# Performance work log

Hardware: AMD Instinct MI355X
Metric: run time of the kernel (lower is better)

The kernel has to match this reference:

```python
import jax, jax.numpy as jnp
import numpy as np
from jax import lax

B, V, C, D, H, W = 1, 5, 32, 48, 128, 160
RATIO = 8


def setup_inputs() -> dict:
    key = jax.random.key(0)
    k1, k2, k3 = jax.random.split(key, 3)
    features = jax.random.normal(k1, (V, B, C, H, W), jnp.float32)
    # proj_matrices[b, v, 0] = 4x4 extrinsic, proj_matrices[b, v, 1, :3, :3] = intrinsic K
    f = 200.0
    K = np.array([[f, 0.0, W / 2.0], [0.0, f, H / 2.0], [0.0, 0.0, 1.0]], np.float32)
    proj = np.zeros((B, V, 2, 4, 4), np.float32)
    for v in range(V):
        E = np.eye(4, dtype=np.float32)
        E[0, 3] = 2.0 * v  # horizontal baseline per source view
        proj[:, v, 0] = E
        P1 = np.eye(4, dtype=np.float32)
        P1[:3, :3] = K
        proj[:, v, 1] = P1
    proj_matrices = jnp.asarray(proj)
    depth_values = jnp.broadcast_to(jnp.linspace(425.0, 935.0, D, dtype=jnp.float32), (B, D))
    mask = jax.random.normal(k2, (B, 9 * RATIO * RATIO, H, W), jnp.float32)
    W_reg = jax.random.normal(k3, (1, C, 3, 3, 3), jnp.float32) * 0.05
    return {"features": features, "proj_matrices": proj_matrices,
            "depth_values": depth_values, "mask": mask, "W_reg": W_reg}


def _combine(p):
    # p: [B,2,4,4] -> K @ E[:3,:4] written into top 3 rows of extrinsic (as in source)
    top = jnp.einsum('bij,bjk->bik', p[:, 1, :3, :3], p[:, 0, :3, :4])
    return p[:, 0].at[:, :3, :4].set(top)


def _bilinear_sample(src, x, y):
    # src [B,C,H,W]; x,y [B,P] pixel coords; zeros padding, align_corners=True
    Bs, Cs, Hs, Ws = src.shape
    x0 = jnp.floor(x)
    y0 = jnp.floor(y)
    wx = x - x0
    wy = y - y0
    src_flat = src.reshape(Bs, Cs, Hs * Ws)

    def gather(xi, yi, w):
        valid = (xi >= 0) & (xi <= Ws - 1) & (yi >= 0) & (yi <= Hs - 1)
        xi_c = jnp.clip(xi, 0, Ws - 1).astype(jnp.int32)
        yi_c = jnp.clip(yi, 0, Hs - 1).astype(jnp.int32)
        idx = (yi_c * Ws + xi_c)[:, None, :]
        vals = jnp.take_along_axis(src_flat, jnp.broadcast_to(idx, (Bs, Cs, idx.shape[-1])), axis=2)
        return vals * (w * valid)[:, None, :]

    return (gather(x0, y0, (1 - wx) * (1 - wy)) + gather(x0 + 1, y0, wx * (1 - wy))
            + gather(x0, y0 + 1, (1 - wx) * wy) + gather(x0 + 1, y0 + 1, wx * wy))


def _homo_warp(src_fea, src_proj, ref_proj, depth_values):
    # faithful homo_warping2: project ref pixel grid at each depth hypothesis into src view
    Bs, Cs, Hs, Ws = src_fea.shape
    Dd = depth_values.shape[1]
    proj = jnp.einsum('bij,bjk->bik', src_proj, jnp.linalg.inv(ref_proj))
    rot = proj[:, :3, :3]
    trans = proj[:, :3, 3]
    ys, xs = jnp.meshgrid(jnp.arange(Hs, dtype=src_fea.dtype), jnp.arange(Ws, dtype=src_fea.dtype), indexing='ij')
    xyz = jnp.stack([xs.ravel(), ys.ravel(), jnp.ones(Hs * Ws, dtype=src_fea.dtype)])  # [3,HW]
    rot_xyz = jnp.einsum('bij,jp->bip', rot, xyz)  # [B,3,HW]
    pts = rot_xyz[:, :, None, :] * depth_values[:, None, :, None] + trans[:, :, None, None]  # [B,3,D,HW]
    gx = pts[:, 0] / pts[:, 2]
    gy = pts[:, 1] / pts[:, 2]
    warped = _bilinear_sample(src_fea, gx.reshape(Bs, -1), gy.reshape(Bs, -1))
    return warped.reshape(Bs, Cs, Dd, Hs, Ws)


def _convex_upsample(depth, mask, r):
    # depth [N,1,H,W], mask [N,9*r*r,H,W] -> [N, r*H, r*W]
    N, _, Hh, Ww = depth.shape
    m = jax.nn.softmax(mask.reshape(N, 1, 9, r, r, Hh, Ww), axis=2)
    dp = jnp.pad(depth, ((0, 0), (0, 0), (1, 1), (1, 1)))
    nb = jnp.stack([dp[:, :, dy:dy + Hh, dx:dx + Ww] for dy in range(3) for dx in range(3)], axis=2)
    up = jnp.sum(m * nb[:, :, :, None, None], axis=2)  # [N,1,r,r,H,W]
    up = up.transpose(0, 1, 4, 2, 5, 3)  # [N,1,H,r,W,r]
    return up.reshape(N, r * Hh, r * Ww)


def reference(features, proj_matrices, depth_values, mask, W_reg):
    num_views = features.shape[0]
    Dd = depth_values.shape[1]
    ref_proj = _combine(proj_matrices[:, 0])
    # variance cost-volume accumulation over views (ref volume broadcast along D)
    vsum = features[0][:, :, None, :, :]
    vsq = vsum ** 2
    for v in range(1, num_views):
        src_proj = _combine(proj_matrices[:, v])
        wv = _homo_warp(features[v], src_proj, ref_proj, depth_values)
        vsum = vsum + wv
        vsq = vsq + wv * wv
    variance = vsq / num_views - (vsum / num_views) ** 2  # [B,C,D,H,W]
    # cost regularization stand-in: 3x3x3 conv C->1, SAME padding
    pre = lax.conv_general_dilated(variance, W_reg, (1, 1, 1), 'SAME',
                                   dimension_numbers=('NCDHW', 'OIDHW', 'NCDHW'))[:, 0]
    prob = jax.nn.softmax(pre, axis=1)  # [B,D,H,W]
    depth = jnp.sum(prob * depth_values[:, :, None, None], axis=1)  # [B,H,W]
    # photometric confidence (no-grad path): sliding sum of 4 along D, pad (1,2)
    pd = jnp.pad(prob, ((0, 0), (1, 2), (0, 0), (0, 0)))
    sum4 = pd[:, 0:Dd] + pd[:, 1:Dd + 1] + pd[:, 2:Dd + 2] + pd[:, 3:Dd + 3]
    di = jnp.sum(prob * jnp.arange(Dd, dtype=prob.dtype)[None, :, None, None], axis=1).astype(jnp.int32)
    di = jnp.clip(di, 0, Dd - 1)
    conf = jax.lax.stop_gradient(jnp.take_along_axis(sum4, di[:, None], axis=1)[:, 0])
    depth_up = _convex_upsample(depth[:, None], mask, RATIO)
    return (depth_up, depth, conf)
```

## Files before the change

### kernel.cpp

```cpp
#include <hip/hip_runtime.h>
#include <hip/hip_bf16.h>


#define NV 5
#define NC 32
#define ND 48
#define NH 128
#define NW 160
#define HW (NH * NW)
#define DHW (ND * HW)

typedef __attribute__((ext_vector_type(2))) float f32x2;
typedef __attribute__((ext_vector_type(4))) float f32x4;
typedef __attribute__((ext_vector_type(2), aligned(4))) float f32x2u;

#define OFF_M      0
#define OFF_WF     256
#define OFF_DEPTHF 4096
#define OFF_PRE    86016
#define OFF_WV     4018176

__global__ void k_setup(const float* __restrict__ proj,
                        const float* __restrict__ wreg,
                        float* __restrict__ M, float* __restrict__ wf) {
  if (threadIdx.x != 0) return;
  double P[NV][2][4][4];
  for (int v = 0; v < NV; ++v)
    for (int m = 0; m < 2; ++m)
      for (int i = 0; i < 4; ++i)
        for (int j = 0; j < 4; ++j)
          P[v][m][i][j] = (double)proj[((v * 2 + m) * 4 + i) * 4 + j];
  double C[NV][4][4];
  for (int v = 0; v < NV; ++v) {
    for (int i = 0; i < 4; ++i)
      for (int j = 0; j < 4; ++j) C[v][i][j] = P[v][0][i][j];
    for (int i = 0; i < 3; ++i)
      for (int j = 0; j < 4; ++j) {
        double s = 0.0;
        for (int k = 0; k < 3; ++k) s += P[v][1][i][k] * P[v][0][k][j];
        C[v][i][j] = s;
      }
  }
  double a[4][8];
  for (int i = 0; i < 4; ++i)
    for (int j = 0; j < 4; ++j) { a[i][j] = C[0][i][j]; a[i][j + 4] = (i == j) ? 1.0 : 0.0; }
  for (int col = 0; col < 4; ++col) {
    int piv = col; double best = fabs(a[col][col]);
    for (int r = col + 1; r < 4; ++r) { double v = fabs(a[r][col]); if (v > best) { best = v; piv = r; } }
    if (piv != col)
      for (int j = 0; j < 8; ++j) { double t = a[col][j]; a[col][j] = a[piv][j]; a[piv][j] = t; }
    double pv = a[col][col];
    for (int j = 0; j < 8; ++j) a[col][j] /= pv;
    for (int r = 0; r < 4; ++r) if (r != col) {
      double f = a[r][col];
      for (int j = 0; j < 8; ++j) a[r][j] -= f * a[col][j];
    }
  }
  double inv[4][4];
  for (int i = 0; i < 4; ++i)
    for (int j = 0; j < 4; ++j) inv[i][j] = a[i][j + 4];
  for (int v = 1; v < NV; ++v) {
    float* m = M + (v - 1) * 12;
    for (int i = 0; i < 3; ++i) {
      double r[4] = {0, 0, 0, 0};
      for (int k = 0; k < 4; ++k) {
        double cv = C[v][i][k];
        for (int j = 0; j < 4; ++j) r[j] += cv * inv[k][j];
      }
      m[i * 3 + 0] = (float)r[0]; m[i * 3 + 1] = (float)r[1]; m[i * 3 + 2] = (float)r[2];
      m[9 + i] = (float)r[3];
    }
  }
  for (int c = 0; c < NC; ++c) {
    for (int t = 0; t < 27; ++t) wf[c * 28 + t] = wreg[c * 27 + t];
    wf[c * 28 + 27] = 0.f;
  }
}

__global__ __launch_bounds__(256) void k_warpvar(
    const float* __restrict__ feat,
    const float* __restrict__ depthv,
    const float* __restrict__ M,
    const float* __restrict__ wf,
    __hip_bfloat16* __restrict__ WV)
{
  int idx = blockIdx.x * 256 + threadIdx.x;
  int x = idx % NW;
  int t1 = idx / NW;
  int y = t1 % NH;
  int d = t1 / NH;
  int pix = y * NW + x;
  float xf = (float)x, yf = (float)y;
  float df = depthv[d];

  int   off[4];
  float wA[4], wB[4];
  bool any4 = false;

#pragma unroll
  for (int v = 0; v < 4; ++v) {
    const float* m = M + v * 12;
    float rx = m[0] * xf + m[1] * yf + m[2];
    float ry = m[3] * xf + m[4] * yf + m[5];
    float rz = m[6] * xf + m[7] * yf + m[8];
    float px = rx * df + m[9];
    float py = ry * df + m[10];
    float pz = rz * df + m[11];
    float gx = px / pz;
    float gy = py / pz;
    float y0 = floorf(gy);
    float wy = gy - y0;
    bool two = (wy == 0.f) || (wy == 1.f);
    any4 = any4 || !two;
    float rowf = (wy == 0.f) ? y0 : (y0 + 1.f);
    float x0 = floorf(gx);
    float wx = gx - x0;
    bool yok  = (rowf >= 0.f) && (rowf <= (float)(NH - 1));
    bool x0ok = (x0 >= 0.f) && (x0 <= (float)(NW - 1)) && yok;
    bool x1ok = (x0 + 1.f >= 0.f) && (x0 + 1.f <= (float)(NW - 1)) && yok;
    float rc = fminf(fmaxf(rowf, 0.f), (float)(NH - 1));
    float xc = fminf(fmaxf(x0, 0.f), (float)(NW - 1));
    int xi = (int)xc;
    int o = (int)rc * NW + xi;
    bool ddv = (o == HW - 1);
    bool sv  = (x0 >= 0.f) && (xi <= NW - 2);
    o -= ddv ? 1 : 0;
    float w0 = (1.f - wx) * (x0ok ? 1.f : 0.f);
    float w1 = wx * (x1ok ? 1.f : 0.f);
    float wsum = w0 + w1;
    wA[v] = ddv ? 0.f : (sv ? w0 : wsum);
    wB[v] = ddv ? wsum : (sv ? w1 : 0.f);
    off[v] = o;
  }

  f32x2 wv[14];
#pragma unroll
  for (int u = 0; u < 14; ++u) { wv[u].x = 0.f; wv[u].y = 0.f; }

  if (__builtin_expect(any4, 0)) {
    int cidx[16]; float cw[16];
#pragma unroll
    for (int v = 0; v < 4; ++v) {
      const float* m = M + v * 12;
      float rx = m[0] * xf + m[1] * yf + m[2];
      float ry = m[3] * xf + m[4] * yf + m[5];
      float rz = m[6] * xf + m[7] * yf + m[8];
      float px = rx * df + m[9];
      float py = ry * df + m[10];
      float pz = rz * df + m[11];
      float gx = px / pz;
      float gy = py / pz;
      float x0 = floorf(gx), y0 = floorf(gy);
      float wx = gx - x0, wy = gy - y0;
      float cxs[2] = {x0, x0 + 1.f}, cys[2] = {y0, y0 + 1.f};
      float wxs[2] = {1.f - wx, wx}, wys[2] = {1.f - wy, wy};
#pragma unroll
      for (int cy = 0; cy < 2; ++cy)
#pragma unroll
        for (int cx = 0; cx < 2; ++cx) {
          float fx = cxs[cx], fy = cys[cy];
          bool valid = (fx >= 0.f) && (fx <= (float)(NW - 1)) &&
                       (fy >= 0.f) && (fy <= (float)(NH - 1));
          float fxc = fminf(fmaxf(fx, 0.f), (float)(NW - 1));
          float fyc = fminf(fmaxf(fy, 0.f), (float)(NH - 1));
          int xi2 = (int)fxc, yi2 = (int)fyc;
          cidx[v * 4 + cy * 2 + cx] = yi2 * NW + xi2;
          cw[v * 4 + cy * 2 + cx] = wxs[cx] * wys[cy] * (valid ? 1.f : 0.f);
        }
    }
    for (int c = 0; c < NC; ++c) {
      float f0 = feat[c * HW + pix];
      float vs = f0, vq = f0 * f0;
#pragma unroll
      for (int v = 0; v < 4; ++v) {
        const float* fv = feat + ((v + 1) * NC + c) * HW;
        float val = cw[v * 4 + 0] * fv[cidx[v * 4 + 0]]
                  + cw[v * 4 + 1] * fv[cidx[v * 4 + 1]]
                  + cw[v * 4 + 2] * fv[cidx[v * 4 + 2]]
                  + cw[v * 4 + 3] * fv[cidx[v * 4 + 3]];
        vs += val;
        vq += val * val;
      }
      float var = vq * 0.2f - (vs * 0.2f) * (vs * 0.2f);
      const f32x2* wrow = (const f32x2*)(wf + c * 28);
      f32x2 vv; vv.x = var; vv.y = var;
#pragma unroll
      for (int u = 0; u < 14; ++u) wv[u] += wrow[u] * vv;
    }
  } else {
#pragma unroll
    for (int c = 0; c < NC; ++c) {
      float f0 = feat[c * HW + pix];
      float vs = f0, vq = f0 * f0;
#pragma unroll
      for (int v = 0; v < 4; ++v) {
        const float* fv = feat + ((v + 1) * NC + c) * HW;
        f32x2u e = *(const f32x2u*)(fv + off[v]);
        float val = wA[v] * e.x + wB[v] * e.y;
        vs += val;
        vq += val * val;
      }
      float var = vq * 0.2f - (vs * 0.2f) * (vs * 0.2f);
      const f32x2* wrow = (const f32x2*)(wf + c * 28);
      f32x2 vv; vv.x = var; vv.y = var;
#pragma unroll
      for (int u = 0; u < 14; ++u) wv[u] += wrow[u] * vv;
    }
  }

#pragma unroll
  for (int u = 0; u < 14; ++u) {
    int t0 = 2 * u;
    WV[t0 * DHW + idx] = __float2bfloat16(wv[u].x);
    if (t0 + 1 < 27) WV[(t0 + 1) * DHW + idx] = __float2bfloat16(wv[u].y);
  }
}

__global__ __launch_bounds__(256) void k_conv(const __hip_bfloat16* __restrict__ WV,
                                              float* __restrict__ pre) {
  int idx = blockIdx.x * 256 + threadIdx.x;
  int x = idx % NW;
  int t1 = idx / NW;
  int y = t1 % NH;
  int d = t1 / NH;
  float acc = 0.f;
#pragma unroll
  for (int dd = 0; dd < 3; ++dd) {
    int dp = d + dd - 1;
    bool dok = (dp >= 0) && (dp < ND);
    int dpc = min(max(dp, 0), ND - 1);
#pragma unroll
    for (int i = 0; i < 3; ++i) {
      int yp = y + i - 1;
      bool yok = (yp >= 0) && (yp < NH);
      int ypc = min(max(yp, 0), NH - 1);
#pragma unroll
      for (int j = 0; j < 3; ++j) {
        int xp = x + j - 1;
        bool xok = (xp >= 0) && (xp < NW);
        int xpc = min(max(xp, 0), NW - 1);
        int t = dd * 9 + i * 3 + j;
        float v = __bfloat162float(WV[t * DHW + dpc * HW + ypc * NW + xpc]);
        acc += (dok && yok && xok) ? v : 0.f;
      }
    }
  }
  pre[idx] = acc;
}

__global__ __launch_bounds__(256) void k_softmax(const float* __restrict__ pre,
                                                 const float* __restrict__ depthv,
                                                 float* __restrict__ depthf,
                                                 float* __restrict__ out_depth,
                                                 float* __restrict__ out_conf) {
  int p = blockIdx.x * 256 + threadIdx.x;
  float pr[ND];
  float m = -1e30f;
#pragma unroll
  for (int d = 0; d < ND; ++d) { pr[d] = pre[d * HW + p]; m = fmaxf(m, pr[d]); }
  float s = 0.f;
#pragma unroll
  for (int d = 0; d < ND; ++d) { pr[d] = expf(pr[d] - m); s += pr[d]; }
  float inv = 1.f / s;
  float dep = 0.f, ti = 0.f;
#pragma unroll
  for (int d = 0; d < ND; ++d) {
    float prob = pr[d] * inv;
    pr[d] = prob;
    dep += prob * depthv[d];
    ti += prob * (float)d;
  }
  int di = (int)ti;
  di = di < 0 ? 0 : (di > ND - 1 ? ND - 1 : di);
  float conf = 0.f;
#pragma unroll
  for (int d = 0; d < ND; ++d)
    conf += (d >= di - 1 && d <= di + 2) ? pr[d] : 0.f;
  depthf[p] = dep;
  out_depth[p] = dep;
  out_conf[p] = conf;
}

__global__ __launch_bounds__(256) void k_upsample(const float* __restrict__ mask,
                                                  const float* __restrict__ depthf,
                                                  float* __restrict__ out) {
  int idx = blockIdx.x * 256 + threadIdx.x;
  int x = idx % NW;
  int r = idx / NW;
  int y = r % NH;
  int dy = r / NH;
  int pix = y * NW + x;

  float dv[9];
#pragma unroll
  for (int k = 0; k < 9; ++k) {
    int ky = y + k / 3 - 1;
    int kx = x + k % 3 - 1;
    bool ok = (ky >= 0) && (ky < NH) && (kx >= 0) && (kx < NW);
    int kyc = min(max(ky, 0), NH - 1);
    int kxc = min(max(kx, 0), NW - 1);
    float t = depthf[kyc * NW + kxc];
    dv[k] = ok ? t : 0.f;
  }

  float res[8];
#pragma unroll
  for (int dx = 0; dx < 8; ++dx) {
    float mv[9];
    float mmax = -1e30f;
#pragma unroll
    for (int k = 0; k < 9; ++k) {
      mv[k] = mask[(size_t)(k * 64 + dy * 8 + dx) * HW + pix];
      mmax = fmaxf(mmax, mv[k]);
    }
    float s = 0.f, acc = 0.f;
#pragma unroll
    for (int k = 0; k < 9; ++k) {
      float e = expf(mv[k] - mmax);
      s += e;
      acc += e * dv[k];
    }
    res[dx] = acc / s;
  }

  float* op = out + (size_t)(y * 8 + dy) * (NW * 8) + x * 8;
  f32x4 lo, hi;
  lo.x = res[0]; lo.y = res[1]; lo.z = res[2]; lo.w = res[3];
  hi.x = res[4]; hi.y = res[5]; hi.z = res[6]; hi.w = res[7];
  *(f32x4*)op = lo;
  *(f32x4*)(op + 4) = hi;
}

extern "C" void kernel_launch(void* const* d_in, const int* in_sizes, int n_in,
                              void* d_out, int out_size, void* d_ws, size_t ws_size,
                              hipStream_t stream) {
  const float* feat   = (const float*)d_in[0];
  const float* proj   = (const float*)d_in[1];
  const float* depthv = (const float*)d_in[2];
  const float* mask   = (const float*)d_in[3];
  const float* wreg   = (const float*)d_in[4];

  char* ws = (char*)d_ws;
  float* M       = (float*)(ws + OFF_M);
  float* wf      = (float*)(ws + OFF_WF);
  float* depthf  = (float*)(ws + OFF_DEPTHF);
  float* pre     = (float*)(ws + OFF_PRE);
  __hip_bfloat16* WV = (__hip_bfloat16*)(ws + OFF_WV);

  float* out = (float*)d_out;
  float* out_depth = out + (NH * 8) * (NW * 8);
  float* out_conf  = out_depth + HW;

  k_setup<<<1, 64, 0, stream>>>(proj, wreg, M, wf);
  k_warpvar<<<DHW / 256, 256, 0, stream>>>(feat, depthv, M, wf, WV);
  k_conv<<<DHW / 256, 256, 0, stream>>>(WV, pre);
  k_softmax<<<HW / 256, 256, 0, stream>>>(pre, depthv, depthf, out_depth, out_conf);
  k_upsample<<<(NH * 8 * NW * 8 / 8) / 256, 256, 0, stream>>>(mask, depthf, out);
}
```

Measured before the change: 241.3 us.

## Vectorize conv to eight outputs per thread and batch warp gathers

The 27-tap gather conv now computes eight consecutive x outputs per thread. It uses 16-byte bf16 vector loads per tap plane plus edge halo words, shares loads across neighbouring outputs, and writes the results with float4 stores. This cuts per-element load instructions and index arithmetic. The warp/variance kernel's two-tap path now issues all gathers for eight channels before doing the math, to expose memory-level parallelism. The price is higher register pressure and less parallelism in the conv grid.

```diff
diff --git a/kernel.cpp b/kernel.cpp
--- a/kernel.cpp
+++ b/kernel.cpp
@@ -13,12 +13,20 @@
 typedef __attribute__((ext_vector_type(2))) float f32x2;
 typedef __attribute__((ext_vector_type(4))) float f32x4;
 typedef __attribute__((ext_vector_type(2), aligned(4))) float f32x2u;
+typedef __attribute__((ext_vector_type(8))) unsigned short u16x8;
 
 #define OFF_M      0
 #define OFF_WF     256
 #define OFF_DEPTHF 4096
 #define OFF_PRE    86016
 #define OFF_WV     4018176
+
+__device__ __forceinline__ float bf2f(unsigned short u) {
+  uint32_t b = ((uint32_t)u) << 16;
+  float f;
+  __builtin_memcpy(&f, &b, 4);
+  return f;
+}
 
 __global__ void k_setup(const float* __restrict__ proj,
                         const float* __restrict__ wreg,
@@ -117,7 +125,7 @@
     float wx = gx - x0;
     bool yok  = (rowf >= 0.f) && (rowf <= (float)(NH - 1));
     bool x0ok = (x0 >= 0.f) && (x0 <= (float)(NW - 1)) && yok;
-    bool x1ok = (x0 + 1.f >= 0.f) && (x0 + 1.f <= (float)(NW - 1)) && yok;
+    bool x1ok = (x0 >= -1.f) && (x0 <= (float)(NW - 2)) && yok;
     float rc = fminf(fmaxf(rowf, 0.f), (float)(NH - 1));
     float xc = fminf(fmaxf(x0, 0.f), (float)(NW - 1));
     int xi = (int)xc;
@@ -189,22 +197,36 @@
     }
   } else {
 #pragma unroll
-    for (int c = 0; c < NC; ++c) {
-      float f0 = feat[c * HW + pix];
-      float vs = f0, vq = f0 * f0;
-#pragma unroll
-      for (int v = 0; v < 4; ++v) {
-        const float* fv = feat + ((v + 1) * NC + c) * HW;
-        f32x2u e = *(const f32x2u*)(fv + off[v]);
-        float val = wA[v] * e.x + wB[v] * e.y;
-        vs += val;
-        vq += val * val;
+    for (int g = 0; g < NC; g += 8) {
+      float f0[8];
+      f32x2 e[8][4];
+#pragma unroll
+      for (int cc = 0; cc < 8; ++cc) {
+        int c = g + cc;
+        f0[cc] = feat[c * HW + pix];
+#pragma unroll
+        for (int v = 0; v < 4; ++v) {
+          const float* fv = feat + ((v + 1) * NC + c) * HW;
+          f32x2u t = *(const f32x2u*)(fv + off[v]);
+          e[cc][v].x = t.x; e[cc][v].y = t.y;
+        }
       }
-      float var = vq * 0.2f - (vs * 0.2f) * (vs * 0.2f);
-      const f32x2* wrow = (const f32x2*)(wf + c * 28);
-      f32x2 vv; vv.x = var; vv.y = var;
-#pragma unroll
-      for (int u = 0; u < 14; ++u) wv[u] += wrow[u] * vv;
+#pragma unroll
+      for (int cc = 0; cc < 8; ++cc) {
+        int c = g + cc;
+        float vs = f0[cc], vq = f0[cc] * f0[cc];
+#pragma unroll
+        for (int v = 0; v < 4; ++v) {
+          float val = wA[v] * e[cc][v].x + wB[v] * e[cc][v].y;
+          vs += val;
+          vq += val * val;
+        }
+        float var = vq * 0.2f - (vs * 0.2f) * (vs * 0.2f);
+        const f32x2* wrow = (const f32x2*)(wf + c * 28);
+        f32x2 vv; vv.x = var; vv.y = var;
+#pragma unroll
+        for (int u = 0; u < 14; ++u) wv[u] += wrow[u] * vv;
+      }
     }
   }
 
@@ -218,12 +240,21 @@
 
 __global__ __launch_bounds__(256) void k_conv(const __hip_bfloat16* __restrict__ WV,
                                               float* __restrict__ pre) {
-  int idx = blockIdx.x * 256 + threadIdx.x;
-  int x = idx % NW;
-  int t1 = idx / NW;
-  int y = t1 % NH;
-  int d = t1 / NH;
-  float acc = 0.f;
+  int t8 = blockIdx.x * 256 + threadIdx.x;
+  int x8 = (t8 % (NW / 8)) * 8;
+  int r = t8 / (NW / 8);
+  int y = r % NH;
+  int d = r / NH;
+
+  bool lo_ok = (x8 > 0);
+  bool hi_ok = (x8 < NW - 8);
+  int xlo = lo_ok ? x8 - 2 : 0;
+  int xhi = hi_ok ? x8 + 8 : NW - 8;
+
+  float acc[8];
+#pragma unroll
+  for (int k = 0; k < 8; ++k) acc[k] = 0.f;
+
 #pragma unroll
   for (int dd = 0; dd < 3; ++dd) {
     int dp = d + dd - 1;
@@ -234,18 +265,33 @@
       int yp = y + i - 1;
       bool yok = (yp >= 0) && (yp < NH);
       int ypc = min(max(yp, 0), NH - 1);
-#pragma unroll
-      for (int j = 0; j < 3; ++j) {
-        int xp = x + j - 1;
-        bool xok = (xp >= 0) && (xp < NW);
-        int xpc = min(max(xp, 0), NW - 1);
-        int t = dd * 9 + i * 3 + j;
-        float v = __bfloat162float(WV[t * DHW + dpc * HW + ypc * NW + xpc]);
-        acc += (dok && yok && xok) ? v : 0.f;
-      }
-    }
-  }
-  pre[idx] = acc;
+      float gok = (dok && yok) ? 1.f : 0.f;
+      const __hip_bfloat16* base =
+          WV + (size_t)(dd * 9 + i * 3) * DHW + (size_t)dpc * HW + ypc * NW;
+
+      u16x8 m0 = *(const u16x8*)(base + x8);
+      uint32_t l0; __builtin_memcpy(&l0, base + xlo, 4);
+      u16x8 m1 = *(const u16x8*)(base + DHW + x8);
+      u16x8 m2 = *(const u16x8*)(base + 2 * (size_t)DHW + x8);
+      uint32_t h2; __builtin_memcpy(&h2, base + 2 * (size_t)DHW + xhi, 4);
+
+      float em1 = lo_ok ? bf2f((unsigned short)(l0 >> 16)) : 0.f;
+      float e8  = hi_ok ? bf2f((unsigned short)(h2 & 0xffff)) : 0.f;
+
+      acc[0] += gok * (em1 + bf2f(m1[0]) + bf2f(m2[1]));
+#pragma unroll
+      for (int k = 1; k < 7; ++k)
+        acc[k] += gok * (bf2f(m0[k - 1]) + bf2f(m1[k]) + bf2f(m2[k + 1]));
+      acc[7] += gok * (bf2f(m0[6]) + bf2f(m1[7]) + e8);
+    }
+  }
+
+  float* op = pre + (size_t)d * HW + y * NW + x8;
+  f32x4 lo4, hi4;
+  lo4.x = acc[0]; lo4.y = acc[1]; lo4.z = acc[2]; lo4.w = acc[3];
+  hi4.x = acc[4]; hi4.y = acc[5]; hi4.z = acc[6]; hi4.w = acc[7];
+  *(f32x4*)op = lo4;
+  *(f32x4*)(op + 4) = hi4;
 }
 
 __global__ __launch_bounds__(256) void k_softmax(const float* __restrict__ pre,
@@ -353,7 +399,7 @@
 
   k_setup<<<1, 64, 0, stream>>>(proj, wreg, M, wf);
   k_warpvar<<<DHW / 256, 256, 0, stream>>>(feat, depthv, M, wf, WV);
-  k_conv<<<DHW / 256, 256, 0, stream>>>(WV, pre);
+  k_conv<<<(DHW / 8) / 256, 256, 0, stream>>>(WV, pre);
   k_softmax<<<HW / 256, 256, 0, stream>>>(pre, depthv, depthf, out_depth, out_conf);
   k_upsample<<<(NH * 8 * NW * 8 / 8) / 256, 256, 0, stream>>>(mask, depthf, out);
 }
```

New measurement: 225.0 us. 1.07x faster.

## Software-pipeline warpvar channel loads and split upsample into two-column threads

Applied to the files above, without the earlier changes.

In the fast path of k_warpvar, the 32-channel loop becomes eight groups of four channels. Loads for the next group are double-buffered and issued before the current group is computed, with sched_barrier fences to keep the compiler from reordering, so gather latency is meant to overlap with FMA work. k_upsample now uses four times as many threads, each producing two output columns instead of eight, which adds parallelism and gives more coalesced mask reads at the cost of recomputing the 3x3 depth neighbourhood per thread. The x1ok bound check is also rewritten in an equivalent form.

```diff
diff --git a/kernel.cpp b/kernel.cpp
--- a/kernel.cpp
+++ b/kernel.cpp
@@ -77,6 +77,47 @@
   }
 }
 
+struct Grp {
+  float f0[4];
+  f32x2 e[4][4];
+};
+
+__device__ __forceinline__ void loadg(const float* __restrict__ feat, int pix,
+                                      const int* off, int g, Grp& r) {
+#pragma unroll
+  for (int cc = 0; cc < 4; ++cc) {
+    int c = g * 4 + cc;
+    r.f0[cc] = feat[c * HW + pix];
+#pragma unroll
+    for (int v = 0; v < 4; ++v) {
+      const float* fv = feat + ((v + 1) * NC + c) * HW;
+      f32x2u t = *(const f32x2u*)(fv + off[v]);
+      r.e[cc][v].x = t.x; r.e[cc][v].y = t.y;
+    }
+  }
+}
+
+__device__ __forceinline__ void compg(const float* __restrict__ wf,
+                                      const float* wA, const float* wB,
+                                      int g, const Grp& r, f32x2* wv) {
+#pragma unroll
+  for (int cc = 0; cc < 4; ++cc) {
+    int c = g * 4 + cc;
+    float vs = r.f0[cc], vq = r.f0[cc] * r.f0[cc];
+#pragma unroll
+    for (int v = 0; v < 4; ++v) {
+      float val = wA[v] * r.e[cc][v].x + wB[v] * r.e[cc][v].y;
+      vs += val;
+      vq += val * val;
+    }
+    float var = vq * 0.2f - (vs * 0.2f) * (vs * 0.2f);
+    const f32x2* wrow = (const f32x2*)(wf + c * 28);
+    f32x2 vv; vv.x = var; vv.y = var;
+#pragma unroll
+    for (int u = 0; u < 14; ++u) wv[u] += wrow[u] * vv;
+  }
+}
+
 __global__ __launch_bounds__(256) void k_warpvar(
     const float* __restrict__ feat,
     const float* __restrict__ depthv,
@@ -117,7 +158,7 @@
     float wx = gx - x0;
     bool yok  = (rowf >= 0.f) && (rowf <= (float)(NH - 1));
     bool x0ok = (x0 >= 0.f) && (x0 <= (float)(NW - 1)) && yok;
-    bool x1ok = (x0 + 1.f >= 0.f) && (x0 + 1.f <= (float)(NW - 1)) && yok;
+    bool x1ok = (x0 >= -1.f) && (x0 <= (float)(NW - 2)) && yok;
     float rc = fminf(fmaxf(rowf, 0.f), (float)(NH - 1));
     float xc = fminf(fmaxf(x0, 0.f), (float)(NW - 1));
     int xi = (int)xc;
@@ -188,24 +229,31 @@
       for (int u = 0; u < 14; ++u) wv[u] += wrow[u] * vv;
     }
   } else {
-#pragma unroll
-    for (int c = 0; c < NC; ++c) {
-      float f0 = feat[c * HW + pix];
-      float vs = f0, vq = f0 * f0;
-#pragma unroll
-      for (int v = 0; v < 4; ++v) {
-        const float* fv = feat + ((v + 1) * NC + c) * HW;
-        f32x2u e = *(const f32x2u*)(fv + off[v]);
-        float val = wA[v] * e.x + wB[v] * e.y;
-        vs += val;
-        vq += val * val;
-      }
-      float var = vq * 0.2f - (vs * 0.2f) * (vs * 0.2f);
-      const f32x2* wrow = (const f32x2*)(wf + c * 28);
-      f32x2 vv; vv.x = var; vv.y = var;
-#pragma unroll
-      for (int u = 0; u < 14; ++u) wv[u] += wrow[u] * vv;
-    }
+    Grp A, B;
+    loadg(feat, pix, off, 0, A);
+    loadg(feat, pix, off, 1, B);
+    __builtin_amdgcn_sched_barrier(0);
+    compg(wf, wA, wB, 0, A, wv);
+    loadg(feat, pix, off, 2, A);
+    __builtin_amdgcn_sched_barrier(0);
+    compg(wf, wA, wB, 1, B, wv);
+    loadg(feat, pix, off, 3, B);
+    __builtin_amdgcn_sched_barrier(0);
+    compg(wf, wA, wB, 2, A, wv);
+    loadg(feat, pix, off, 4, A);
+    __builtin_amdgcn_sched_barrier(0);
+    compg(wf, wA, wB, 3, B, wv);
+    loadg(feat, pix, off, 5, B);
+    __builtin_amdgcn_sched_barrier(0);
+    compg(wf, wA, wB, 4, A, wv);
+    loadg(feat, pix, off, 6, A);
+    __builtin_amdgcn_sched_barrier(0);
+    compg(wf, wA, wB, 5, B, wv);
+    loadg(feat, pix, off, 7, B);
+    __builtin_amdgcn_sched_barrier(0);
+    compg(wf, wA, wB, 6, A, wv);
+    __builtin_amdgcn_sched_barrier(0);
+    compg(wf, wA, wB, 7, B, wv);
   }
 
 #pragma unroll
@@ -285,11 +333,12 @@
                                                   const float* __restrict__ depthf,
                                                   float* __restrict__ out) {
   int idx = blockIdx.x * 256 + threadIdx.x;
-  int x = idx % NW;
-  int r = idx / NW;
-  int y = r % NH;
-  int dy = r / NH;
-  int pix = y * NW + x;
+  int pix = idx % HW;
+  int g = idx / HW;
+  int dy = g >> 2;
+  int dx0 = (g & 3) * 2;
+  int x = pix % NW;
+  int y = pix / NW;
 
   float dv[9];
 #pragma unroll
@@ -303,9 +352,10 @@
     dv[k] = ok ? t : 0.f;
   }
 
-  float res[8];
-#pragma unroll
-  for (int dx = 0; dx < 8; ++dx) {
+  float res[2];
+#pragma unroll
+  for (int j = 0; j < 2; ++j) {
+    int dx = dx0 + j;
     float mv[9];
     float mmax = -1e30f;
 #pragma unroll
@@ -320,15 +370,12 @@
       s += e;
       acc += e * dv[k];
     }
-    res[dx] = acc / s;
-  }
-
-  float* op = out + (size_t)(y * 8 + dy) * (NW * 8) + x * 8;
-  f32x4 lo, hi;
-  lo.x = res[0]; lo.y = res[1]; lo.z = res[2]; lo.w = res[3];
-  hi.x = res[4]; hi.y = res[5]; hi.z = res[6]; hi.w = res[7];
-  *(f32x4*)op = lo;
-  *(f32x4*)(op + 4) = hi;
+    res[j] = acc / s;
+  }
+
+  float* op = out + (size_t)(y * 8 + dy) * (NW * 8) + x * 8 + dx0;
+  f32x2 r2; r2.x = res[0]; r2.y = res[1];
+  *(f32x2*)op = r2;
 }
 
 extern "C" void kernel_launch(void* const* d_in, const int* in_sizes, int n_in,
@@ -355,5 +402,5 @@
   k_warpvar<<<DHW / 256, 256, 0, stream>>>(feat, depthv, M, wf, WV);
   k_conv<<<DHW / 256, 256, 0, stream>>>(WV, pre);
   k_softmax<<<HW / 256, 256, 0, stream>>>(pre, depthv, depthf, out_depth, out_conf);
-  k_upsample<<<(NH * 8 * NW * 8 / 8) / 256, 256, 0, stream>>>(mask, depthf, out);
-}
+  k_upsample<<<(HW * 32) / 256, 256, 0, stream>>>(mask, depthf, out);
+}
```

Measured after the change: 227.4 us. 1.06x faster.

## Split warp-variance from channel contraction and run contraction on bf16 MFMA

Applied to the files above, without the earlier changes.

The warp kernel now writes per-voxel 32-channel variance as packed bf16 (64 bytes per voxel) instead of doing the 27-tap channel contraction in scalar FMAs. A new kernel does the channel-to-tap contraction with 16x16x32 bf16 MFMA instructions and writes the tap-major WV buffer. Feature loads are also batched in groups of 8 channels to raise memory-level parallelism. This adds an extra kernel launch and a round trip of roughly 63 MB of intermediate traffic, and rounds the variance to bf16 before the contraction, which loses some precision.

```diff
diff --git a/kernel.cpp b/kernel.cpp
--- a/kernel.cpp
+++ b/kernel.cpp
@@ -13,16 +13,28 @@
 typedef __attribute__((ext_vector_type(2))) float f32x2;
 typedef __attribute__((ext_vector_type(4))) float f32x4;
 typedef __attribute__((ext_vector_type(2), aligned(4))) float f32x2u;
+typedef __attribute__((ext_vector_type(8))) short short8;
+typedef __attribute__((ext_vector_type(4))) unsigned int u32x4;
 
 #define OFF_M      0
-#define OFF_WF     256
+#define OFF_WFB    256
 #define OFF_DEPTHF 4096
 #define OFF_PRE    86016
 #define OFF_WV     4018176
+#define OFF_VAR    57102336
+
+__device__ __forceinline__ uint32_t pack_bf16(float a, float b) {
+  __hip_bfloat16 ba = __float2bfloat16(a), bb = __float2bfloat16(b);
+  uint16_t ua, ub;
+  __builtin_memcpy(&ua, &ba, 2);
+  __builtin_memcpy(&ub, &bb, 2);
+  return (uint32_t)ua | ((uint32_t)ub << 16);
+}
 
 __global__ void k_setup(const float* __restrict__ proj,
                         const float* __restrict__ wreg,
-                        float* __restrict__ M, float* __restrict__ wf) {
+                        float* __restrict__ M,
+                        unsigned short* __restrict__ wfB) {
   if (threadIdx.x != 0) return;
   double P[NV][2][4][4];
   for (int v = 0; v < NV; ++v)
@@ -71,18 +83,23 @@
       m[9 + i] = (float)r[3];
     }
   }
-  for (int c = 0; c < NC; ++c) {
-    for (int t = 0; t < 27; ++t) wf[c * 28 + t] = wreg[c * 27 + t];
-    wf[c * 28 + 27] = 0.f;
-  }
-}
-
-__global__ __launch_bounds__(256) void k_warpvar(
+  for (int nt = 0; nt < 2; ++nt)
+    for (int l = 0; l < 64; ++l)
+      for (int e = 0; e < 8; ++e) {
+        int tap = nt * 16 + (l & 15);
+        int k = (l >> 4) * 8 + e;
+        float val = (tap < 27) ? wreg[k * 27 + tap] : 0.f;
+        __hip_bfloat16 b = __float2bfloat16(val);
+        uint16_t u; __builtin_memcpy(&u, &b, 2);
+        wfB[(nt * 64 + l) * 8 + e] = u;
+      }
+}
+
+__global__ __launch_bounds__(256) void k_warpvar_lite(
     const float* __restrict__ feat,
     const float* __restrict__ depthv,
     const float* __restrict__ M,
-    const float* __restrict__ wf,
-    __hip_bfloat16* __restrict__ WV)
+    unsigned short* __restrict__ varO)
 {
   int idx = blockIdx.x * 256 + threadIdx.x;
   int x = idx % NW;
@@ -117,7 +134,7 @@
     float wx = gx - x0;
     bool yok  = (rowf >= 0.f) && (rowf <= (float)(NH - 1));
     bool x0ok = (x0 >= 0.f) && (x0 <= (float)(NW - 1)) && yok;
-    bool x1ok = (x0 + 1.f >= 0.f) && (x0 + 1.f <= (float)(NW - 1)) && yok;
+    bool x1ok = (x0 >= -1.f) && (x0 <= (float)(NW - 2)) && yok;
     float rc = fminf(fmaxf(rowf, 0.f), (float)(NH - 1));
     float xc = fminf(fmaxf(x0, 0.f), (float)(NW - 1));
     int xi = (int)xc;
@@ -133,11 +150,41 @@
     off[v] = o;
   }
 
-  f32x2 wv[14];
-#pragma unroll
-  for (int u = 0; u < 14; ++u) { wv[u].x = 0.f; wv[u].y = 0.f; }
-
-  if (__builtin_expect(any4, 0)) {
+  uint32_t st[16];
+
+  if (__builtin_expect(!any4, 1)) {
+#pragma unroll
+    for (int g = 0; g < NC; g += 8) {
+      float f0[8];
+      f32x2 e[8][4];
+#pragma unroll
+      for (int cc = 0; cc < 8; ++cc) {
+        int c = g + cc;
+        f0[cc] = feat[c * HW + pix];
+#pragma unroll
+        for (int v = 0; v < 4; ++v) {
+          const float* fv = feat + ((v + 1) * NC + c) * HW;
+          f32x2u t = *(const f32x2u*)(fv + off[v]);
+          e[cc][v].x = t.x; e[cc][v].y = t.y;
+        }
+      }
+      float vr[8];
+#pragma unroll
+      for (int cc = 0; cc < 8; ++cc) {
+        float vs = f0[cc], vq = f0[cc] * f0[cc];
+#pragma unroll
+        for (int v = 0; v < 4; ++v) {
+          float val = wA[v] * e[cc][v].x + wB[v] * e[cc][v].y;
+          vs += val;
+          vq += val * val;
+        }
+        vr[cc] = vq * 0.2f - (vs * 0.2f) * (vs * 0.2f);
+      }
+#pragma unroll
+      for (int q = 0; q < 4; ++q)
+        st[g / 2 + q] = pack_bf16(vr[2 * q], vr[2 * q + 1]);
+    }
+  } else {
     int cidx[16]; float cw[16];
 #pragma unroll
     for (int v = 0; v < 4; ++v) {
@@ -168,51 +215,69 @@
           cw[v * 4 + cy * 2 + cx] = wxs[cx] * wys[cy] * (valid ? 1.f : 0.f);
         }
     }
-    for (int c = 0; c < NC; ++c) {
-      float f0 = feat[c * HW + pix];
-      float vs = f0, vq = f0 * f0;
-#pragma unroll
-      for (int v = 0; v < 4; ++v) {
-        const float* fv = feat + ((v + 1) * NC + c) * HW;
-        float val = cw[v * 4 + 0] * fv[cidx[v * 4 + 0]]
-                  + cw[v * 4 + 1] * fv[cidx[v * 4 + 1]]
-                  + cw[v * 4 + 2] * fv[cidx[v * 4 + 2]]
-                  + cw[v * 4 + 3] * fv[cidx[v * 4 + 3]];
-        vs += val;
-        vq += val * val;
-      }
-      float var = vq * 0.2f - (vs * 0.2f) * (vs * 0.2f);
-      const f32x2* wrow = (const f32x2*)(wf + c * 28);
-      f32x2 vv; vv.x = var; vv.y = var;
-#pragma unroll
-      for (int u = 0; u < 14; ++u) wv[u] += wrow[u] * vv;
-    }
-  } else {
-#pragma unroll
-    for (int c = 0; c < NC; ++c) {
-      float f0 = feat[c * HW + pix];
-      float vs = f0, vq = f0 * f0;
-#pragma unroll
-      for (int v = 0; v < 4; ++v) {
-        const float* fv = feat + ((v + 1) * NC + c) * HW;
-        f32x2u e = *(const f32x2u*)(fv + off[v]);
-        float val = wA[v] * e.x + wB[v] * e.y;
-        vs += val;
-        vq += val * val;
-      }
-      float var = vq * 0.2f - (vs * 0.2f) * (vs * 0.2f);
-      const f32x2* wrow = (const f32x2*)(wf + c * 28);
-      f32x2 vv; vv.x = var; vv.y = var;
-#pragma unroll
-      for (int u = 0; u < 14; ++u) wv[u] += wrow[u] * vv;
-    }
-  }
-
-#pragma unroll
-  for (int u = 0; u < 14; ++u) {
-    int t0 = 2 * u;
-    WV[t0 * DHW + idx] = __float2bfloat16(wv[u].x);
-    if (t0 + 1 < 27) WV[(t0 + 1) * DHW + idx] = __float2bfloat16(wv[u].y);
+    for (int g = 0; g < NC; g += 2) {
+      float vr[2];
+#pragma unroll
+      for (int cc = 0; cc < 2; ++cc) {
+        int c = g + cc;
+        float f0 = feat[c * HW + pix];
+        float vs = f0, vq = f0 * f0;
+#pragma unroll
+        for (int v = 0; v < 4; ++v) {
+          const float* fv = feat + ((v + 1) * NC + c) * HW;
+          float val = cw[v * 4 + 0] * fv[cidx[v * 4 + 0]]
+                    + cw[v * 4 + 1] * fv[cidx[v * 4 + 1]]
+                    + cw[v * 4 + 2] * fv[cidx[v * 4 + 2]]
+                    + cw[v * 4 + 3] * fv[cidx[v * 4 + 3]];
+          vs += val;
+          vq += val * val;
+        }
+        vr[cc] = vq * 0.2f - (vs * 0.2f) * (vs * 0.2f);
+      }
+      st[g / 2] = pack_bf16(vr[0], vr[1]);
+    }
+  }
+
+  u32x4* dst = (u32x4*)((uint32_t*)varO + (size_t)idx * 16);
+#pragma unroll
+  for (int q = 0; q < 4; ++q) {
+    u32x4 o4;
+    o4.x = st[4 * q + 0]; o4.y = st[4 * q + 1];
+    o4.z = st[4 * q + 2]; o4.w = st[4 * q + 3];
+    dst[q] = o4;
+  }
+}
+
+__global__ __launch_bounds__(256) void k_contract(
+    const unsigned short* __restrict__ varI,
+    const unsigned short* __restrict__ wfB,
+    unsigned short* __restrict__ WVu)
+{
+  int tid = threadIdx.x;
+  int lane = tid & 63;
+  int wavebase = blockIdx.x * 256 + (tid & ~63);
+  short8 bfr0 = *(const short8*)(wfB + (size_t)lane * 8);
+  short8 bfr1 = *(const short8*)(wfB + (size_t)(64 + lane) * 8);
+  int lr = lane & 15, lk = lane >> 4;
+  uint32_t* W32 = (uint32_t*)WVu;
+
+#pragma unroll
+  for (int m = 0; m < 4; ++m) {
+    int voxA = wavebase + m * 16 + lr;
+    short8 af = *(const short8*)(varI + (size_t)voxA * 32 + lk * 8);
+    f32x4 z = {0.f, 0.f, 0.f, 0.f};
+    f32x4 a0 = __builtin_amdgcn_mfma_f32_16x16x32_bf16(af, bfr0, z, 0, 0, 0);
+    f32x4 a1 = __builtin_amdgcn_mfma_f32_16x16x32_bf16(af, bfr1, z, 0, 0, 0);
+    int v4 = wavebase + m * 16 + lk * 4;
+    size_t o0 = ((size_t)lr * DHW + v4) >> 1;
+    W32[o0] = pack_bf16(a0[0], a0[1]);
+    W32[o0 + 1] = pack_bf16(a0[2], a0[3]);
+    int tap1 = 16 + lr;
+    if (tap1 < 27) {
+      size_t o1 = ((size_t)tap1 * DHW + v4) >> 1;
+      W32[o1] = pack_bf16(a1[0], a1[1]);
+      W32[o1 + 1] = pack_bf16(a1[2], a1[3]);
+    }
   }
 }
 
@@ -342,17 +407,20 @@
 
   char* ws = (char*)d_ws;
   float* M       = (float*)(ws + OFF_M);
-  float* wf      = (float*)(ws + OFF_WF);
+  unsigned short* wfB = (unsigned short*)(ws + OFF_WFB);
   float* depthf  = (float*)(ws + OFF_DEPTHF);
   float* pre     = (float*)(ws + OFF_PRE);
-  __hip_bfloat16* WV = (__hip_bfloat16*)(ws + OFF_WV);
+  unsigned short* WVu = (unsigned short*)(ws + OFF_WV);
+  unsigned short* varB = (unsigned short*)(ws + OFF_VAR);
+  const __hip_bfloat16* WV = (const __hip_bfloat16*)(ws + OFF_WV);
 
   float* out = (float*)d_out;
   float* out_depth = out + (NH * 8) * (NW * 8);
   float* out_conf  = out_depth + HW;
 
-  k_setup<<<1, 64, 0, stream>>>(proj, wreg, M, wf);
-  k_warpvar<<<DHW / 256, 256, 0, stream>>>(feat, depthv, M, wf, WV);
+  k_setup<<<1, 64, 0, stream>>>(proj, wreg, M, wfB);
+  k_warpvar_lite<<<DHW / 256, 256, 0, stream>>>(feat, depthv, M, varB);
+  k_contract<<<DHW / 256, 256, 0, stream>>>(varB, wfB, WVu);
   k_conv<<<DHW / 256, 256, 0, stream>>>(WV, pre);
   k_softmax<<<HW / 256, 256, 0, stream>>>(pre, depthv, depthf, out_depth, out_conf);
   k_upsample<<<(NH * 8 * NW * 8 / 8) / 256, 256, 0, stream>>>(mask, depthf, out);
```

Result: slower. 306.4 us (+27.0%).
